# Optimization experiments

Hardware: AMD Instinct MI355X
Metric: run time of the kernel (lower is better)

Reference implementation:

```python
import jax, jax.numpy as jnp
import numpy as np

SEG_LENS = (2048, 4096, 8192)
DIL_RATES = (1, 2, 4)
DIM = 1024
HEADS = 16
HEAD_DIM = DIM // HEADS
BATCH = 1
SEQ = sum(SEG_LENS)


def _hilbert_perm(L):
    """Permutation ordering the first L row-major cells of a 2^k x 2^k grid by Hilbert distance."""
    n = 1
    while n * n < L:
        n *= 2
    idx = np.arange(n * n, dtype=np.int64)
    x = idx % n
    y = idx // n
    d = np.zeros(n * n, dtype=np.int64)
    s = n // 2
    while s > 0:
        rx = ((x & s) > 0).astype(np.int64)
        ry = ((y & s) > 0).astype(np.int64)
        d += s * s * ((3 * rx) ^ ry)
        swap = ry == 0
        flip = swap & (rx == 1)
        x = np.where(flip, s - 1 - x, x)
        y = np.where(flip, s - 1 - y, y)
        x, y = np.where(swap, y, x), np.where(swap, x, y)
        s //= 2
    return np.argsort(d[:L], kind='stable')


def _segment_attn(x_seg, wqkv, bqkv, wo, bo, rate, use_hilbert=True):
    """HilbertAttentionCore: hilbert reorder -> QKV -> dilated attention -> out proj -> inverse reorder.
    x_seg: [B, L, D] -> [B, L, D]
    """
    B, L, D = x_seg.shape
    hd = D // HEADS
    perm_np = _hilbert_perm(L)
    perm = jnp.asarray(perm_np)
    inv = jnp.asarray(np.argsort(perm_np))
    xh = x_seg[:, perm] if use_hilbert else x_seg
    qkv = xh @ wqkv + bqkv                      # [B, L, 3D]
    q, k, v = jnp.split(qkv, 3, axis=-1)
    q = q.reshape(B, L, HEADS, hd)
    k = k.reshape(B, L, HEADS, hd)
    v = v.reshape(B, L, HEADS, hd)
    Lr = L // rate
    offs = jnp.arange(HEADS) % rate             # per-head dilation offset
    hidx = jnp.arange(HEADS)

    def dilate(t):
        # position i = off + rate*j  <->  reshape(L//rate, rate)[j, off]
        tr = t.reshape(B, Lr, rate, HEADS, hd)
        return tr[:, :, offs, hidx, :]          # [B, Lr, H, hd]

    qd, kd, vd = dilate(q), dilate(k), dilate(v)
    scale = 1.0 / np.sqrt(hd).astype(np.float32)
    scores = jnp.einsum('bihd,bjhd->bhij', qd, kd) * scale
    probs = jax.nn.softmax(scores, axis=-1)
    od = jnp.einsum('bhij,bjhd->bihd', probs, vd)  # [B, Lr, H, hd]
    # scatter each head's dilated subsequence back; uncovered (head,pos) stay zero
    outr = jnp.zeros((B, Lr, rate, HEADS, hd), x_seg.dtype)
    outr = outr.at[:, :, offs, hidx, :].set(od)
    out = outr.reshape(B, L, HEADS * hd) @ wo + bo
    return out[:, inv] if use_hilbert else out


def setup_inputs() -> dict:
    key = jax.random.key(0)
    ks = jax.random.split(key, 16)
    inp = {
        'q': jax.random.normal(ks[0], (BATCH, SEQ, HEADS, HEAD_DIM), jnp.float32),
        'k': jax.random.normal(ks[1], (BATCH, SEQ, HEADS, HEAD_DIM), jnp.float32),
        'v': jax.random.normal(ks[2], (BATCH, SEQ, HEADS, HEAD_DIM), jnp.float32),
    }
    for i in range(3):
        inp[f'wqkv_{i}'] = jax.random.normal(ks[3 + 4 * i], (DIM, 3 * DIM), jnp.float32) * 0.02
        inp[f'bqkv_{i}'] = jnp.zeros((3 * DIM,), jnp.float32)
        inp[f'wo_{i}'] = jax.random.normal(ks[4 + 4 * i], (DIM, DIM), jnp.float32) * 0.02
        inp[f'bo_{i}'] = jnp.zeros((DIM,), jnp.float32)
    return inp


def reference(q, k, v,
              wqkv_0, bqkv_0, wo_0, bo_0,
              wqkv_1, bqkv_1, wo_1, bo_1,
              wqkv_2, bqkv_2, wo_2, bo_2):
    B, S, H, hd = q.shape
    x = q.reshape(B, S, H * hd)  # single-GPU path uses q only (as in the source)
    params = [(wqkv_0, bqkv_0, wo_0, bo_0),
              (wqkv_1, bqkv_1, wo_1, bo_1),
              (wqkv_2, bqkv_2, wo_2, bo_2)]
    outs = []
    pos = 0
    for (seg_len, rate), (wq, bq, wo, bo) in zip(zip(SEG_LENS, DIL_RATES), params):
        if pos >= S:
            break
        end = min(pos + seg_len, S)
        outs.append(_segment_attn(x[:, pos:end], wq, bq, wo, bo, rate))
        pos = end
    return jnp.concatenate(outs, axis=1).reshape(B, S, H, hd)
```

## Files before the change

kernel.cpp:

```cpp
#include <hip/hip_runtime.h>
#include <stdint.h>
#include <stddef.h>

typedef unsigned short u16;
typedef short bf16x8 __attribute__((ext_vector_type(8)));
typedef float f32x4 __attribute__((ext_vector_type(4)));
typedef float f32x16 __attribute__((ext_vector_type(16)));
typedef unsigned short ushort8v __attribute__((ext_vector_type(8)));
typedef int i32x2 __attribute__((ext_vector_type(2)));

#define LR 2048
#define LOG2E 1.44269504088896f

__device__ __forceinline__ u16 f2bf(float f) {
  unsigned u = __float_as_uint(f);
  unsigned r = u + 0x7fffu + ((u >> 16) & 1u);
  return (u16)(r >> 16);
}

__device__ __forceinline__ unsigned cvtpk(float lo, float hi) {
  unsigned r;
  asm("v_cvt_pk_bf16_f32 %0, %1, %2" : "=v"(r) : "v"(lo), "v"(hi));
  return r;
}

__device__ __forceinline__ void plswap(unsigned& a, unsigned& b) {
#if __has_builtin(__builtin_amdgcn_permlane32_swap)
  i32x2 r = __builtin_amdgcn_permlane32_swap((int)a, (int)b, false, false);
  a = (unsigned)r[0];
  b = (unsigned)r[1];
#else
  asm volatile("s_nop 1\n\tv_permlane32_swap_b32 %0, %1\n\ts_nop 1"
               : "+v"(a), "+v"(b));
#endif
}
__device__ __forceinline__ float xhalf_sum(float x) {
  unsigned a = __float_as_uint(x), b = __float_as_uint(x);
  plswap(a, b);
  return __uint_as_float(a) + __uint_as_float(b);
}

__device__ __forceinline__ void gl_lds16(const void* g, void* l) {
  __builtin_amdgcn_global_load_lds((__attribute__((address_space(1))) void*)g,
                                   (__attribute__((address_space(3))) void*)l,
                                   16, 0, 0);
}

__global__ void hilbert_kernel(int* __restrict__ perm) {
  int idx = blockIdx.x * 256 + threadIdx.x;
  if (idx >= 14336) return;
  int seg = (idx < 2048) ? 0 : (idx < 6144 ? 1 : 2);
  int segpos = (seg == 0) ? 0 : (seg == 1 ? 2048 : 6144);
  int L = 2048 << seg;
  int n = (seg == 2) ? 128 : 64;
  int t = idx - segpos;
  int d = (L == n * n) ? t : ((t < (L >> 1)) ? t : t + L);
  int x = 0, y = 0;
  for (int s = 1; s < n; s <<= 1) {
    int rx = 1 & (d >> 1);
    int ry = 1 & (d ^ rx);
    if (ry == 0) {
      if (rx == 1) { x = s - 1 - x; y = s - 1 - y; }
      int tmp = x; x = y; y = tmp;
    }
    x += s * rx; y += s * ry;
    d >>= 2;
  }
  perm[idx] = y * n + x;
}

__global__ void wtrans_kernel(const float* __restrict__ q0, const float* __restrict__ q1,
                              const float* __restrict__ q2, const float* __restrict__ o0,
                              const float* __restrict__ o1, const float* __restrict__ o2,
                              u16* __restrict__ dq, u16* __restrict__ dw) {
  const int seg = blockIdx.z;
  const int bx = blockIdx.x;
  const int K = 1024;
  int tx = threadIdx.x, ty = threadIdx.y;
  __shared__ float tl[32][33];
  const float* S;
  u16* D;
  int N, n0, do_remap;
  if (bx < 96) {
    S = (seg == 0) ? q0 : (seg == 1 ? q1 : q2);
    D = dq + (size_t)seg * K * 3072;
    N = 3072; n0 = bx * 32; do_remap = 0;
  } else {
    S = (seg == 0) ? o0 : (seg == 1 ? o1 : o2);
    D = dw + (size_t)seg * K * 1024;
    N = 1024; n0 = (bx - 96) * 32; do_remap = 1;
  }
  int k0 = blockIdx.y * 32;
  #pragma unroll
  for (int i = 0; i < 4; i++)
    tl[ty + 8 * i][tx] = S[(size_t)(k0 + ty + 8 * i) * N + n0 + tx];
  __syncthreads();
  int kk = k0 + tx;
  if (do_remap) {
    int rate = 1 << seg;
    int h = kk >> 6;
    int h2 = (h & (rate - 1)) * (16 >> seg) + (h >> seg);
    kk = h2 * 64 + (kk & 63);
  }
  #pragma unroll
  for (int i = 0; i < 4; i++)
    D[(size_t)(n0 + ty + 8 * i) * K + kk] = f2bf(tl[tx][ty + 8 * i]);
}

__global__ void gather_kernel(const float* __restrict__ x, const int* __restrict__ perm,
                              u16* __restrict__ xh) {
  int rr = blockIdx.x;
  int seg = (rr < 2048) ? 0 : (rr < 6144 ? 1 : 2);
  int segpos = (seg == 0) ? 0 : (seg == 1 ? 2048 : 6144);
  int rate = 1 << seg;
  int rl = rr - segpos;
  int t = (rl & (LR - 1)) * rate + (rl >> 11);
  int orig = segpos + perm[segpos + t];
  float4 v = *((const float4*)(x + (size_t)orig * 1024) + threadIdx.x);
  ushort4 o;
  o.x = f2bf(v.x); o.y = f2bf(v.y); o.z = f2bf(v.z); o.w = f2bf(v.w);
  *((ushort4*)(xh + (size_t)rr * 1024) + threadIdx.x) = o;
}

__global__ __launch_bounds__(512, 2) void qkv_gemm_kernel(
    const u16* __restrict__ A, const u16* __restrict__ Bt,
    const float* __restrict__ b0, const float* __restrict__ b1,
    const float* __restrict__ b2, u16* __restrict__ C) {
  __shared__ char smem[131072];
  const int tid = threadIdx.x;
  const int lane = tid & 63, wid = tid >> 6;
  const int wm = wid >> 2, wn = wid & 3;
  const int bid = blockIdx.x;
  const int xcd = bid & 7;
  const int idx = bid >> 3;
  const int grp = idx / 42;
  const int rem = idx % 42;
  const int rb = xcd * 7 + rem / 6;
  const int nb = grp * 6 + rem % 6;
  const int seg = (rb < 8) ? 0 : (rb < 24 ? 1 : 2);
  const float* bias = (seg == 0) ? b0 : (seg == 1 ? b1 : b2);
  const size_t arow0 = (size_t)rb * 256;
  const char* Ab = (const char*)(A + arow0 * 1024);
  const char* Bb = (const char*)(Bt + ((size_t)seg * 3072 + (size_t)nb * 256) * 1024);

  f32x4 acc[8][4] = {};

  #pragma unroll
  for (int it = 0; it < 4; it++) {
    int p = (it * 512 + tid) * 16;
    int e = p ^ (((p >> 7) & 7) << 4);
    int row = e >> 7, col = e & 127;
    gl_lds16(Ab + (size_t)row * 2048 + col, smem + it * 8192 + wid * 1024);
    gl_lds16(Bb + (size_t)row * 2048 + col, smem + 65536 + it * 8192 + wid * 1024);
  }
  __syncthreads();

  for (int kt = 0; kt < 16; kt++) {
    const int buf = kt & 1, nbuf = buf ^ 1;
    char* As = smem + buf * 32768;
    char* Bs = smem + 65536 + buf * 32768;
    if (kt < 15) {
      #pragma unroll
      for (int it = 0; it < 4; it++) {
        int p = (it * 512 + tid) * 16;
        int e = p ^ (((p >> 7) & 7) << 4);
        int row = e >> 7, col = e & 127;
        gl_lds16(Ab + (size_t)row * 2048 + (kt + 1) * 128 + col,
                 smem + nbuf * 32768 + it * 8192 + wid * 1024);
        gl_lds16(Bb + (size_t)row * 2048 + (kt + 1) * 128 + col,
                 smem + 65536 + nbuf * 32768 + it * 8192 + wid * 1024);
      }
    }
    #pragma unroll
    for (int kc = 0; kc < 2; kc++) {
      bf16x8 af[8], bfr[4];
      #pragma unroll
      for (int m = 0; m < 8; m++) {
        int row = wm * 128 + m * 16 + (lane & 15);
        int e = row * 128 + kc * 64 + ((lane >> 4) << 4);
        af[m] = *(const bf16x8*)(As + (e ^ ((row & 7) << 4)));
      }
      #pragma unroll
      for (int n = 0; n < 4; n++) {
        int row = wn * 64 + n * 16 + (lane & 15);
        int e = row * 128 + kc * 64 + ((lane >> 4) << 4);
        bfr[n] = *(const bf16x8*)(Bs + (e ^ ((row & 7) << 4)));
      }
      #pragma unroll
      for (int m = 0; m < 8; m++)
        #pragma unroll
        for (int n = 0; n < 4; n++)
          acc[m][n] = __builtin_amdgcn_mfma_f32_16x16x32_bf16(af[m], bfr[n], acc[m][n], 0, 0, 0);
    }
    __syncthreads();
  }

  float bv[4];
  #pragma unroll
  for (int n = 0; n < 4; n++) bv[n] = bias[nb * 256 + wn * 64 + n * 16 + (lane & 15)];
  #pragma unroll
  for (int pass = 0; pass < 2; pass++) {
    if (wm == pass) {
      #pragma unroll
      for (int m = 0; m < 8; m++)
        #pragma unroll
        for (int n = 0; n < 4; n++)
          #pragma unroll
          for (int j = 0; j < 4; j++) {
            int r = m * 16 + ((lane >> 4) << 2) + j;
            int c = wn * 64 + n * 16 + (lane & 15);
            *(u16*)(smem + r * 528 + c * 2) = f2bf(acc[m][n][j] + bv[n]);
          }
    }
    __syncthreads();
    #pragma unroll
    for (int it = 0; it < 8; it++) {
      int ci = it * 512 + tid;
      int row = ci >> 5, c16 = ci & 31;
      bf16x8 vv = *(const bf16x8*)(smem + row * 528 + c16 * 16);
      u16* crow = C + (arow0 + pass * 128 + row) * 3072 + nb * 256;
      *(bf16x8*)((char*)crow + c16 * 16) = vv;
    }
    if (pass == 0) __syncthreads();
  }
}

__global__ __launch_bounds__(256) void attn_kernel(const u16* __restrict__ qkv,
                                                   u16* __restrict__ opre) {
  __shared__ char smem[32768];
  const int tid = threadIdx.x;
  const int lane = tid & 63;
  const int wid = tid >> 6;
  const int l31 = lane & 31;
  const int hi = lane >> 5;
  const int by = blockIdx.y;
  const int seg = by >> 4, h = by & 15;
  const int segrow = (seg == 0) ? 0 : (seg == 1 ? 2048 : 6144);
  const int rate = 1 << seg;
  const int off = h & (rate - 1);
  const int base = segrow + off * LR;
  const int h_col = off * (16 >> seg) + (h >> seg);
  const int q0 = blockIdx.x * 128;
  const int qw = q0 + wid * 32;
  const char* qb = (const char*)qkv;

  const int vkey0 = 2 * (tid & 31);
  const int vd0 = (tid >> 5) * 8;

  #pragma unroll
  for (int it = 0; it < 2; it++) {
    int p = (it * 256 + tid) * 16;
    int e = p ^ (((p >> 7) & 7) << 4);
    int row = e >> 7, col = e & 127;
    gl_lds16(qb + (size_t)(base + row) * 6144 + 2048 + h * 128 + col,
             smem + it * 4096 + wid * 1024);
  }
  ushort8v v0r = *(const ushort8v*)(qb + (size_t)(base + vkey0) * 6144 + 4096 + h * 128 + vd0 * 2);
  ushort8v v1r = *(const ushort8v*)(qb + (size_t)(base + vkey0 + 1) * 6144 + 4096 + h * 128 + vd0 * 2);
  bf16x8 qf[4];
  #pragma unroll
  for (int i = 0; i < 4; i++)
    qf[i] = *(const bf16x8*)(qb + (size_t)(base + qw + l31) * 6144 + h * 128 + i * 32 + hi * 16);
  #pragma unroll
  for (int dd = 0; dd < 8; dd++) {
    int d = vd0 + dd;
    unsigned val = (unsigned)(u16)v0r[dd] | ((unsigned)(u16)v1r[dd] << 16);
    int addr = d * 128 + vkey0 * 2;
    *(unsigned*)(smem + 16384 + (addr ^ ((d & 7) << 4))) = val;
  }
  __syncthreads();

  float Lrun = 0.f;
  f32x16 accO0 = {}, accO1 = {};
  const float K1 = 0.125f * LOG2E;
  const float C2 = 4.0f * LOG2E;

  for (int kt = 0; kt < 32; kt++) {
    const int cur = kt & 1;
    const int nxt = cur ^ 1;
    char* Ks  = smem + (cur << 13);
    char* Vt  = smem + 16384 + (cur << 13);
    char* Ksn = smem + (nxt << 13);
    char* Vtn = smem + 16384 + (nxt << 13);
    ushort8v nv0, nv1;
    if (kt < 31) {
      #pragma unroll
      for (int it = 0; it < 2; it++) {
        int p = (it * 256 + tid) * 16;
        int e = p ^ (((p >> 7) & 7) << 4);
        int row = e >> 7, col = e & 127;
        gl_lds16(qb + (size_t)(base + (kt + 1) * 64 + row) * 6144 + 2048 + h * 128 + col,
                 Ksn + it * 4096 + wid * 1024);
      }
      nv0 = *(const ushort8v*)(qb + (size_t)(base + (kt + 1) * 64 + vkey0) * 6144 + 4096 + h * 128 + vd0 * 2);
      nv1 = *(const ushort8v*)(qb + (size_t)(base + (kt + 1) * 64 + vkey0 + 1) * 6144 + 4096 + h * 128 + vd0 * 2);
    }
    #pragma unroll
    for (int s = 0; s < 2; s++) {
      f32x16 sacc = {};
      __builtin_amdgcn_s_setprio(1);
      #pragma unroll
      for (int i = 0; i < 4; i++) {
        int row = s * 32 + l31;
        int addr = (row * 128 + i * 32 + hi * 16) ^ ((row & 7) << 4);
        bf16x8 kf = *(const bf16x8*)(Ks + addr);
        sacc = __builtin_amdgcn_mfma_f32_32x32x16_bf16(kf, qf[i], sacc, 0, 0, 0);
      }
      __builtin_amdgcn_s_setprio(0);
      #pragma unroll
      for (int r = 0; r < 16; r++) sacc[r] = exp2f(sacc[r] * K1 - C2);
      float s8[8];
      #pragma unroll
      for (int t = 0; t < 8; t++) s8[t] = sacc[2 * t] + sacc[2 * t + 1];
      float sm = (((s8[0] + s8[1]) + (s8[2] + s8[3])) + ((s8[4] + s8[5]) + (s8[6] + s8[7])));
      Lrun += xhalf_sum(sm);
      unsigned w[8];
      #pragma unroll
      for (int t = 0; t < 8; t++) w[t] = cvtpk(sacc[2 * t], sacc[2 * t + 1]);
      plswap(w[0], w[2]); plswap(w[1], w[3]);
      plswap(w[4], w[6]); plswap(w[5], w[7]);
      union PU { unsigned u[4]; bf16x8 v; };
      PU pu0, pu1;
      pu0.u[0] = w[0]; pu0.u[1] = w[1]; pu0.u[2] = w[2]; pu0.u[3] = w[3];
      pu1.u[0] = w[4]; pu1.u[1] = w[5]; pu1.u[2] = w[6]; pu1.u[3] = w[7];
      __builtin_amdgcn_s_setprio(1);
      #pragma unroll
      for (int j = 0; j < 2; j++) {
        bf16x8 pa = (j == 0) ? pu0.v : pu1.v;
        #pragma unroll
        for (int dt = 0; dt < 2; dt++) {
          int d = dt * 32 + l31;
          int addr = (d * 128 + s * 64 + j * 32 + hi * 16) ^ ((d & 7) << 4);
          bf16x8 vf = *(const bf16x8*)(Vt + addr);
          if (dt == 0) accO0 = __builtin_amdgcn_mfma_f32_32x32x16_bf16(pa, vf, accO0, 0, 0, 0);
          else         accO1 = __builtin_amdgcn_mfma_f32_32x32x16_bf16(pa, vf, accO1, 0, 0, 0);
        }
      }
      __builtin_amdgcn_s_setprio(0);
    }
    if (kt < 31) {
      #pragma unroll
      for (int dd = 0; dd < 8; dd++) {
        int d = vd0 + dd;
        unsigned val = (unsigned)(u16)nv0[dd] | ((unsigned)(u16)nv1[dd] << 16);
        int addr = d * 128 + vkey0 * 2;
        *(unsigned*)(Vtn + (addr ^ ((d & 7) << 4))) = val;
      }
    }
    __syncthreads();
  }

  float invL = 1.0f / Lrun;
  #pragma unroll
  for (int r = 0; r < 16; r++) {
    int qrow = (r & 3) + 8 * (r >> 2) + 4 * hi;
    float li = __shfl(invL, qrow);
    int qloc = wid * 32 + qrow;
    int a0 = (qloc * 128 + l31 * 2) ^ ((qrow & 7) << 4);
    int a1 = (qloc * 128 + 64 + l31 * 2) ^ ((qrow & 7) << 4);
    *(u16*)(smem + a0) = f2bf(accO0[r] * li);
    *(u16*)(smem + a1) = f2bf(accO1[r] * li);
  }
  __syncthreads();
  #pragma unroll
  for (int it = 0; it < 4; it++) {
    int idx = it * 256 + tid;
    int row = idx >> 3, c16 = idx & 7;
    int a = (row * 128 + c16 * 16) ^ ((row & 7) << 4);
    bf16x8 vv = *(const bf16x8*)(smem + a);
    *(bf16x8*)((char*)(opre + (size_t)(base + q0 + row) * 1024 + h_col * 64) + c16 * 16) = vv;
  }
}

__global__ __launch_bounds__(256) void out_gemm_kernel(
    const u16* __restrict__ A, const u16* __restrict__ Bt,
    const float* __restrict__ b0, const float* __restrict__ b1,
    const float* __restrict__ b2, const int* __restrict__ perm,
    float* __restrict__ Out) {
  __shared__ char smem[65536];
  __shared__ int drow[128];
  const int tid = threadIdx.x;
  const int lane = tid & 63, wid = tid >> 6;
  const int wm = wid >> 1, wn = wid & 1;
  const int rb = blockIdx.x, nb = blockIdx.y;
  const int seg = (rb < 16) ? 0 : (rb < 48 ? 1 : 2);
  const int segpos = (seg == 0) ? 0 : (seg == 1 ? 2048 : 6144);
  const int rate = 1 << seg;
  const float* bias = (seg == 0) ? b0 : (seg == 1 ? b1 : b2);
  const size_t arow0 = (size_t)rb * 128;
  const char* Ab = (const char*)(A + arow0 * 1024);
  const char* Bb = (const char*)(Bt + ((size_t)seg * 1024 + (size_t)nb * 128) * 1024);

  const int blk = (int)(arow0 - segpos) >> 11;
  const int ktpb = 16 >> seg;
  const int kt0 = blk * ktpb;

  f32x4 acc[4][4] = {};

  #pragma unroll
  for (int it = 0; it < 4; it++) {
    int p = (it * 256 + tid) * 16;
    int e = p ^ (((p >> 7) & 7) << 4);
    int row = e >> 7, col = e & 127;
    gl_lds16(Ab + (size_t)row * 2048 + kt0 * 128 + col, smem + it * 4096 + wid * 1024);
    gl_lds16(Bb + (size_t)row * 2048 + kt0 * 128 + col, smem + 32768 + it * 4096 + wid * 1024);
  }
  __syncthreads();

  for (int i = 0; i < ktpb; i++) {
    const int kt = kt0 + i;
    const int buf = i & 1, nbuf = buf ^ 1;
    char* As = smem + buf * 16384;
    char* Bs = smem + 32768 + buf * 16384;
    if (i < ktpb - 1) {
      #pragma unroll
      for (int it = 0; it < 4; it++) {
        int p = (it * 256 + tid) * 16;
        int e = p ^ (((p >> 7) & 7) << 4);
        int row = e >> 7, col = e & 127;
        gl_lds16(Ab + (size_t)row * 2048 + (kt + 1) * 128 + col,
                 smem + nbuf * 16384 + it * 4096 + wid * 1024);
        gl_lds16(Bb + (size_t)row * 2048 + (kt + 1) * 128 + col,
                 smem + 32768 + nbuf * 16384 + it * 4096 + wid * 1024);
      }
    }
    #pragma unroll
    for (int kc = 0; kc < 2; kc++) {
      bf16x8 af[4], bfr[4];
      #pragma unroll
      for (int m = 0; m < 4; m++) {
        int row = wm * 64 + m * 16 + (lane & 15);
        int e = row * 128 + kc * 64 + ((lane >> 4) << 4);
        af[m] = *(const bf16x8*)(As + (e ^ ((row & 7) << 4)));
      }
      #pragma unroll
      for (int n = 0; n < 4; n++) {
        int row = wn * 64 + n * 16 + (lane & 15);
        int e = row * 128 + kc * 64 + ((lane >> 4) << 4);
        bfr[n] = *(const bf16x8*)(Bs + (e ^ ((row & 7) << 4)));
      }
      #pragma unroll
      for (int m = 0; m < 4; m++)
        #pragma unroll
        for (int n = 0; n < 4; n++)
          acc[m][n] = __builtin_amdgcn_mfma_f32_16x16x32_bf16(af[m], bfr[n], acc[m][n], 0, 0, 0);
    }
    __syncthreads();
  }
  if (tid < 128) {
    int rl = (int)arow0 + tid - segpos;
    int t = (rl & (LR - 1)) * rate + (rl >> 11);
    drow[tid] = segpos + perm[segpos + t];
  }
  __syncthreads();
  float bv[4];
  #pragma unroll
  for (int n = 0; n < 4; n++) bv[n] = bias[nb * 128 + wn * 64 + n * 16 + (lane & 15)];
  #pragma unroll
  for (int m = 0; m < 4; m++)
    #pragma unroll
    for (int j = 0; j < 4; j++) {
      int r = wm * 64 + m * 16 + ((lane >> 4) << 2) + j;
      int gr = drow[r];
      float* orow = Out + (size_t)gr * 1024 + nb * 128 + wn * 64;
      #pragma unroll
      for (int n = 0; n < 4; n++)
        orow[n * 16 + (lane & 15)] = acc[m][n][j] + bv[n];
    }
}

extern "C" void kernel_launch(void* const* d_in, const int* in_sizes, int n_in,
                              void* d_out, int out_size, void* d_ws, size_t ws_size,
                              hipStream_t stream) {
  (void)in_sizes; (void)n_in; (void)out_size;
  const float* x = (const float*)d_in[0];
  const float* wqkv0 = (const float*)d_in[3];
  const float* bqkv0 = (const float*)d_in[4];
  const float* wo0 = (const float*)d_in[5];
  const float* bo0 = (const float*)d_in[6];
  const float* wqkv1 = (const float*)d_in[7];
  const float* bqkv1 = (const float*)d_in[8];
  const float* wo1 = (const float*)d_in[9];
  const float* bo1 = (const float*)d_in[10];
  const float* wqkv2 = (const float*)d_in[11];
  const float* bqkv2 = (const float*)d_in[12];
  const float* wo2 = (const float*)d_in[13];
  const float* bo2 = (const float*)d_in[14];

  if (ws_size < 172032000ull) return;
  char* ws = (char*)d_ws;
  int* perm = (int*)ws;
  u16* xh    = (u16*)(ws + 65536);
  u16* wqkvt = (u16*)(ws + 29425664);
  u16* wot   = (u16*)(ws + 48300032);
  u16* qkv   = (u16*)(ws + 54591488);
  u16* opre  = (u16*)(ws + 142671872);
  float* out = (float*)d_out;

  hilbert_kernel<<<56, 256, 0, stream>>>(perm);
  wtrans_kernel<<<dim3(128, 32, 3), dim3(32, 8), 0, stream>>>(wqkv0, wqkv1, wqkv2,
                                                              wo0, wo1, wo2, wqkvt, wot);
  gather_kernel<<<14336, 256, 0, stream>>>(x, perm, xh);
  qkv_gemm_kernel<<<672, 512, 0, stream>>>(xh, wqkvt, bqkv0, bqkv1, bqkv2, qkv);
  attn_kernel<<<dim3(16, 48), 256, 0, stream>>>(qkv, opre);
  out_gemm_kernel<<<dim3(112, 8), 256, 0, stream>>>(opre, wot, bo0, bo1, bo2, perm, out);
}
```

Before: 276.3 us.

## Split attention over two key halves with a separate normalizing combine kernel

The attention grid gains a z dimension that splits the 32 key tiles into two halves of 16. Each block writes unnormalized bf16 partial outputs and per-row softmax denominators, reusing the xh and wqkvt workspace regions as scratch. A new combine kernel adds the two partials and divides by the summed denominators, producing opre in place. This doubles the number of attention blocks to improve CU occupancy and latency hiding. The cost is an extra launch, roughly three full-size bf16 tensors of extra memory traffic, and rounding each partial to bf16 before summing.

```diff
diff --git a/kernel.cpp b/kernel.cpp
--- a/kernel.cpp
+++ b/kernel.cpp
@@ -16,6 +16,9 @@
   unsigned u = __float_as_uint(f);
   unsigned r = u + 0x7fffu + ((u >> 16) & 1u);
   return (u16)(r >> 16);
+}
+__device__ __forceinline__ float bf2f(u16 v) {
+  return __uint_as_float(((unsigned)v) << 16);
 }
 
 __device__ __forceinline__ unsigned cvtpk(float lo, float hi) {
@@ -226,7 +229,9 @@
 }
 
 __global__ __launch_bounds__(256) void attn_kernel(const u16* __restrict__ qkv,
-                                                   u16* __restrict__ opre) {
+                                                   u16* __restrict__ p0,
+                                                   u16* __restrict__ p1,
+                                                   float* __restrict__ Lb) {
   __shared__ char smem[32768];
   const int tid = threadIdx.x;
   const int lane = tid & 63;
@@ -234,6 +239,8 @@
   const int l31 = lane & 31;
   const int hi = lane >> 5;
   const int by = blockIdx.y;
+  const int khalf = blockIdx.z;
+  const int k0 = khalf * 16;
   const int seg = by >> 4, h = by & 15;
   const int segrow = (seg == 0) ? 0 : (seg == 1 ? 2048 : 6144);
   const int rate = 1 << seg;
@@ -243,6 +250,7 @@
   const int q0 = blockIdx.x * 128;
   const int qw = q0 + wid * 32;
   const char* qb = (const char*)qkv;
+  u16* opart = khalf ? p1 : p0;
 
   const int vkey0 = 2 * (tid & 31);
   const int vd0 = (tid >> 5) * 8;
@@ -252,11 +260,11 @@
     int p = (it * 256 + tid) * 16;
     int e = p ^ (((p >> 7) & 7) << 4);
     int row = e >> 7, col = e & 127;
-    gl_lds16(qb + (size_t)(base + row) * 6144 + 2048 + h * 128 + col,
+    gl_lds16(qb + (size_t)(base + k0 * 64 + row) * 6144 + 2048 + h * 128 + col,
              smem + it * 4096 + wid * 1024);
   }
-  ushort8v v0r = *(const ushort8v*)(qb + (size_t)(base + vkey0) * 6144 + 4096 + h * 128 + vd0 * 2);
-  ushort8v v1r = *(const ushort8v*)(qb + (size_t)(base + vkey0 + 1) * 6144 + 4096 + h * 128 + vd0 * 2);
+  ushort8v v0r = *(const ushort8v*)(qb + (size_t)(base + k0 * 64 + vkey0) * 6144 + 4096 + h * 128 + vd0 * 2);
+  ushort8v v1r = *(const ushort8v*)(qb + (size_t)(base + k0 * 64 + vkey0 + 1) * 6144 + 4096 + h * 128 + vd0 * 2);
   bf16x8 qf[4];
   #pragma unroll
   for (int i = 0; i < 4; i++)
@@ -275,7 +283,7 @@
   const float K1 = 0.125f * LOG2E;
   const float C2 = 4.0f * LOG2E;
 
-  for (int kt = 0; kt < 32; kt++) {
+  for (int kt = k0; kt < k0 + 16; kt++) {
     const int cur = kt & 1;
     const int nxt = cur ^ 1;
     char* Ks  = smem + (cur << 13);
@@ -283,7 +291,7 @@
     char* Ksn = smem + (nxt << 13);
     char* Vtn = smem + 16384 + (nxt << 13);
     ushort8v nv0, nv1;
-    if (kt < 31) {
+    if (kt < k0 + 15) {
       #pragma unroll
       for (int it = 0; it < 2; it++) {
         int p = (it * 256 + tid) * 16;
@@ -338,7 +346,7 @@
       }
       __builtin_amdgcn_s_setprio(0);
     }
-    if (kt < 31) {
+    if (kt < k0 + 15) {
       #pragma unroll
       for (int dd = 0; dd < 8; dd++) {
         int d = vd0 + dd;
@@ -350,16 +358,16 @@
     __syncthreads();
   }
 
-  float invL = 1.0f / Lrun;
+  if (hi == 0)
+    Lb[(size_t)khalf * 14336 * 16 + (size_t)(base + qw + l31) * 16 + h_col] = Lrun;
   #pragma unroll
   for (int r = 0; r < 16; r++) {
     int qrow = (r & 3) + 8 * (r >> 2) + 4 * hi;
-    float li = __shfl(invL, qrow);
     int qloc = wid * 32 + qrow;
     int a0 = (qloc * 128 + l31 * 2) ^ ((qrow & 7) << 4);
     int a1 = (qloc * 128 + 64 + l31 * 2) ^ ((qrow & 7) << 4);
-    *(u16*)(smem + a0) = f2bf(accO0[r] * li);
-    *(u16*)(smem + a1) = f2bf(accO1[r] * li);
+    *(u16*)(smem + a0) = f2bf(accO0[r]);
+    *(u16*)(smem + a1) = f2bf(accO1[r]);
   }
   __syncthreads();
   #pragma unroll
@@ -368,8 +376,32 @@
     int row = idx >> 3, c16 = idx & 7;
     int a = (row * 128 + c16 * 16) ^ ((row & 7) << 4);
     bf16x8 vv = *(const bf16x8*)(smem + a);
-    *(bf16x8*)((char*)(opre + (size_t)(base + q0 + row) * 1024 + h_col * 64) + c16 * 16) = vv;
-  }
+    *(bf16x8*)((char*)(opart + (size_t)(base + q0 + row) * 1024 + h_col * 64) + c16 * 16) = vv;
+  }
+}
+
+__global__ __launch_bounds__(128) void combine_kernel(const u16* __restrict__ p0,
+                                                      const u16* __restrict__ p1,
+                                                      const float* __restrict__ Lb,
+                                                      u16* __restrict__ opre) {
+  const int row = blockIdx.x;
+  const int tid = threadIdx.x;
+  __shared__ float sc[16];
+  if (tid < 16) {
+    float l0 = Lb[(size_t)row * 16 + tid];
+    float l1 = Lb[(size_t)14336 * 16 + (size_t)row * 16 + tid];
+    sc[tid] = 1.0f / (l0 + l1);
+  }
+  __syncthreads();
+  int c0 = tid * 8;
+  float scale = sc[c0 >> 6];
+  ushort8v a = *(const ushort8v*)(p0 + (size_t)row * 1024 + c0);
+  ushort8v b = *(const ushort8v*)(p1 + (size_t)row * 1024 + c0);
+  ushort8v o;
+  #pragma unroll
+  for (int i = 0; i < 8; i++)
+    o[i] = f2bf((bf2f((u16)a[i]) + bf2f((u16)b[i])) * scale);
+  *(ushort8v*)(opre + (size_t)row * 1024 + c0) = o;
 }
 
 __global__ __launch_bounds__(256) void out_gemm_kernel(
@@ -495,6 +527,7 @@
   u16* wot   = (u16*)(ws + 48300032);
   u16* qkv   = (u16*)(ws + 54591488);
   u16* opre  = (u16*)(ws + 142671872);
+  float* Lb  = (float*)(ws + 29425664);
   float* out = (float*)d_out;
 
   hilbert_kernel<<<56, 256, 0, stream>>>(perm);
@@ -502,6 +535,7 @@
                                                               wo0, wo1, wo2, wqkvt, wot);
   gather_kernel<<<14336, 256, 0, stream>>>(x, perm, xh);
   qkv_gemm_kernel<<<672, 512, 0, stream>>>(xh, wqkvt, bqkv0, bqkv1, bqkv2, qkv);
-  attn_kernel<<<dim3(16, 48), 256, 0, stream>>>(qkv, opre);
+  attn_kernel<<<dim3(16, 48, 2), 256, 0, stream>>>(qkv, opre, xh, Lb);
+  combine_kernel<<<14336, 128, 0, stream>>>(opre, xh, Lb, opre);
   out_gemm_kernel<<<dim3(112, 8), 256, 0, stream>>>(opre, wot, bo0, bo1, bo2, perm, out);
 }
```

New measurement: 292.2 us. +5.8%, slower.
